# Performance work log

Hardware: AMD Instinct MI355X
Metric: run time of the kernel (lower is better)

Reference implementation:

```python
import jax, jax.numpy as jnp
import numpy as np


def setup_inputs() -> dict:
    key = jax.random.key(0)
    k_idx, k_val = jax.random.split(key)
    XSIZE = 128
    N = 500000
    B = 16
    indices = jax.random.randint(k_idx, (N, 3), 0, XSIZE, dtype=jnp.int32)
    values = jax.random.normal(k_val, (B, N), dtype=jnp.float32)
    return {"indices": indices, "values": values, "xsize": XSIZE}


def reference(indices, values, xsize):
    # densitySmoothnessVolume: scatter-add values into a (B, X, X, X) grid,
    # then TV and MSE smoothness losses over 3-axis finite differences.
    B = values.shape[0]
    X = xsize
    # flat voxel index (z, y, x) -> z*X*X + y*X + x ; shared across batch
    flat = (indices[:, 0].astype(jnp.int32) * X + indices[:, 1]) * X + indices[:, 2]
    grid = jnp.zeros((B, X * X * X), dtype=values.dtype)
    grid = grid.at[:, flat].add(values)  # scatter-add, duplicate indices accumulate
    grid = grid.reshape(B, X, X, X)

    d1 = grid[:, 1:, :, :] - grid[:, :-1, :, :]
    d2 = grid[:, :, 1:, :] - grid[:, :, :-1, :]
    d3 = grid[:, :, :, 1:] - grid[:, :, :, :-1]

    axes = (1, 2, 3)
    # total variation loss, normalized by number of voxels X^3
    num_pixels = jnp.asarray(X * X * X, dtype=values.dtype)
    tv = (jnp.sum(jnp.abs(d1), axis=axes)
          + jnp.sum(jnp.abs(d2), axis=axes)
          + jnp.sum(jnp.abs(d3), axis=axes)) / num_pixels

    # MSE smoothness loss; normalizer replicates TF code exactly:
    # 2 * prod(shape[1:3]) - shape[1] - shape[2] = 2*X^2 - 2*X
    num_pixel_pairs = jnp.asarray(2 * X * X - 2 * X, dtype=values.dtype)
    mse = (jnp.sum(jnp.square(d1), axis=axes)
           + jnp.sum(jnp.square(d2), axis=axes)
           + jnp.sum(jnp.square(d3), axis=axes)) / num_pixel_pairs

    return jnp.stack([tv, mse])  # [2, B]
```

## Files before the change

kernel.cpp:

```cpp
#include <hip/hip_runtime.h>

#define XS 128
#define PLANE (XS * XS)
#define X3 (XS * XS * XS)
#define ZC 4
#define TPB 1024
#define SLOTS 4
#define QPT 4
#define CAP 8192

__device__ __forceinline__ void bar_lgkm() {
    __builtin_amdgcn_sched_barrier(0);
    asm volatile("s_waitcnt lgkmcnt(0)" ::: "memory");
    __builtin_amdgcn_s_barrier();
    __builtin_amdgcn_sched_barrier(0);
}

__global__ __launch_bounds__(256) void init_kernel(
    int* __restrict__ cursor, float* __restrict__ out, int osz)
{
    const int t = threadIdx.x;
    if (t < XS) cursor[t] = 0;
    if (t < osz) out[t] = 0.f;
}

__global__ __launch_bounds__(256) void reorder_kernel(
    const int* __restrict__ idx, int* __restrict__ cursor,
    const float* __restrict__ vals, float* __restrict__ pvT,
    unsigned short* __restrict__ posArr, int N)
{
    __shared__ int lh[XS], lbase[XS];
    const int c0 = blockIdx.x * 1024;
    const int t = threadIdx.x;
    int z[4], key[4];
    int cntm = 0;
    const bool fast = (c0 + 1024 <= N);

    for (int i = t; i < XS; i += 256) lh[i] = 0;

    if (fast) {
        const int4* p = (const int4*)(idx + (size_t)c0 * 3);
        int4 A = p[3 * t], B4 = p[3 * t + 1], C = p[3 * t + 2];
        z[0] = A.x;  key[0] = (A.y << 7) | A.z;
        z[1] = A.w;  key[1] = (B4.x << 7) | B4.y;
        z[2] = B4.z; key[2] = (B4.w << 7) | C.x;
        z[3] = C.y;  key[3] = (C.z << 7) | C.w;
        cntm = 4;
    } else {
        #pragma unroll
        for (int i = 0; i < 4; ++i) {
            const int n = c0 + 4 * t + i;
            if (n < N) {
                z[cntm]   = idx[3 * n];
                key[cntm] = (idx[3 * n + 1] << 7) | idx[3 * n + 2];
                ++cntm;
            }
        }
    }
    __syncthreads();
    #pragma unroll
    for (int i = 0; i < 4; ++i)
        if (i < cntm) atomicAdd(&lh[z[i]], 1);
    __syncthreads();
    for (int i = t; i < XS; i += 256) {
        lbase[i] = lh[i] ? atomicAdd(&cursor[i], lh[i]) : 0;
        lh[i] = 0;
    }
    __syncthreads();

    int slot[4];
    #pragma unroll
    for (int i = 0; i < 4; ++i)
        if (i < cntm) {
            const int r = atomicAdd(&lh[z[i]], 1);
            slot[i] = z[i] * CAP + lbase[z[i]] + r;
            posArr[slot[i]] = (unsigned short)key[i];
        }

    if (fast) {
        float4 vv[16];
        #pragma unroll
        for (int b = 0; b < 16; ++b)
            vv[b] = *(const float4*)(vals + (size_t)b * N + c0 + 4 * t);
        #pragma unroll
        for (int i = 0; i < 4; ++i) {
            float4* dst = (float4*)(pvT + (size_t)slot[i] * 16);
            float4 w0 = make_float4(((const float*)&vv[0])[i],  ((const float*)&vv[1])[i],
                                    ((const float*)&vv[2])[i],  ((const float*)&vv[3])[i]);
            float4 w1 = make_float4(((const float*)&vv[4])[i],  ((const float*)&vv[5])[i],
                                    ((const float*)&vv[6])[i],  ((const float*)&vv[7])[i]);
            float4 w2 = make_float4(((const float*)&vv[8])[i],  ((const float*)&vv[9])[i],
                                    ((const float*)&vv[10])[i], ((const float*)&vv[11])[i]);
            float4 w3 = make_float4(((const float*)&vv[12])[i], ((const float*)&vv[13])[i],
                                    ((const float*)&vv[14])[i], ((const float*)&vv[15])[i]);
            dst[0] = w0; dst[1] = w1; dst[2] = w2; dst[3] = w3;
        }
    } else {
        for (int i = 0; i < cntm; ++i) {
            const int n = c0 + 4 * t + i;
            float* dst = pvT + (size_t)slot[i] * 16;
            for (int b = 0; b < 16; ++b) dst[b] = vals[(size_t)b * N + n];
        }
    }
}

__global__ __launch_bounds__(TPB, 8) void fused_kernel(
    const unsigned short* __restrict__ posArr, const int* __restrict__ cnt,
    const float* __restrict__ pvT, float* __restrict__ out, int Btot)
{
    __shared__ float buf[PLANE];
    __shared__ float rtv[TPB / 64], rms[TPB / 64];

    const int b   = blockIdx.x;
    const int z0  = blockIdx.y * ZC;
    const int tid = threadIdx.x;
    const int pmax = (z0 + ZC < XS) ? (z0 + ZC) : (XS - 1);

    int pos[SLOTS]; float val[SLOTS];
    int pc = 0, ps0 = 0;

    auto prefetch = [&](int zp) {
        ps0 = zp * CAP; pc = cnt[zp];
        #pragma unroll
        for (int i = 0; i < SLOTS; ++i) {
            const int sx = ps0 + tid + i * TPB;
            pos[i] = posArr[sx] & (PLANE - 1);
            val[i] = pvT[(size_t)sx * 16 + b];
        }
    };
    auto scatter = [&]() {
        #pragma unroll
        for (int i = 0; i < SLOTS; ++i) {
            const float v = (tid + i * TPB < pc) ? val[i] : 0.f;
            atomicAdd(&buf[pos[i]], v);
        }
        for (int e = SLOTS * TPB + tid; e < pc; e += TPB) {
            atomicAdd(&buf[posArr[ps0 + e] & (PLANE - 1)],
                      pvT[(size_t)(ps0 + e) * 16 + b]);
        }
    };

    prefetch(z0);
    #pragma unroll
    for (int i = 0; i < QPT; ++i)
        ((float4*)buf)[tid + i * TPB] = make_float4(0.f, 0.f, 0.f, 0.f);
    bar_lgkm();
    scatter();
    prefetch(z0 + 1);
    bar_lgkm();

    float4 prev[QPT];
    float tv = 0.f, ms = 0.f;

    for (int p = z0; p <= pmax; ++p) {
        float4 a[QPT];
        #pragma unroll
        for (int i = 0; i < QPT; ++i)
            a[i] = ((const float4*)buf)[tid + i * TPB];

        if (p > z0) {
            #pragma unroll
            for (int i = 0; i < QPT; ++i) {
                float d;
                d = a[i].x - prev[i].x; tv += fabsf(d); ms += d * d;
                d = a[i].y - prev[i].y; tv += fabsf(d); ms += d * d;
                d = a[i].z - prev[i].z; tv += fabsf(d); ms += d * d;
                d = a[i].w - prev[i].w; tv += fabsf(d); ms += d * d;
            }
        }
        if (p < z0 + ZC) {
            #pragma unroll
            for (int i = 0; i < QPT; ++i) {
                const int q = tid + i * TPB;
                const int qx = q & 31, y = q >> 5;
                float d;
                d = a[i].y - a[i].x; tv += fabsf(d); ms += d * d;
                d = a[i].z - a[i].y; tv += fabsf(d); ms += d * d;
                d = a[i].w - a[i].z; tv += fabsf(d); ms += d * d;
                if (qx < 31) {
                    d = buf[4 * q + 4] - a[i].w; tv += fabsf(d); ms += d * d;
                }
                if (y < XS - 1) {
                    const float4 u = ((const float4*)buf)[q + 32];
                    d = u.x - a[i].x; tv += fabsf(d); ms += d * d;
                    d = u.y - a[i].y; tv += fabsf(d); ms += d * d;
                    d = u.z - a[i].z; tv += fabsf(d); ms += d * d;
                    d = u.w - a[i].w; tv += fabsf(d); ms += d * d;
                }
            }
        }
        #pragma unroll
        for (int i = 0; i < QPT; ++i) prev[i] = a[i];

        if (p < pmax) {
            bar_lgkm();
            #pragma unroll
            for (int i = 0; i < QPT; ++i)
                ((float4*)buf)[tid + i * TPB] = make_float4(0.f, 0.f, 0.f, 0.f);
            bar_lgkm();
            scatter();
            if (p + 2 <= pmax) prefetch(p + 2);
            bar_lgkm();
        }
    }

    for (int o = 32; o > 0; o >>= 1) {
        tv += __shfl_down(tv, o); ms += __shfl_down(ms, o);
    }
    if ((tid & 63) == 0) { rtv[tid >> 6] = tv; rms[tid >> 6] = ms; }
    __syncthreads();
    if (tid == 0) {
        float t = 0.f, m = 0.f;
        #pragma unroll
        for (int w = 0; w < TPB / 64; ++w) { t += rtv[w]; m += rms[w]; }
        atomicAdd(out + b,        t * (1.0f / (float)X3));
        atomicAdd(out + Btot + b, m * (1.0f / (float)(2 * XS * XS - 2 * XS)));
    }
}

extern "C" void kernel_launch(void* const* d_in, const int* in_sizes, int n_in,
                              void* d_out, int out_size, void* d_ws, size_t ws_size,
                              hipStream_t stream)
{
    const int*   indices = (const int*)d_in[0];
    const float* values  = (const float*)d_in[1];
    const int N = in_sizes[0] / 3;
    const int B = in_sizes[1] / N;
    float* out = (float*)d_out;
    char*  ws  = (char*)d_ws;

    float* pvT = (float*)ws;
    unsigned short* posArr = (unsigned short*)(ws + (size_t)XS * CAP * 16 * sizeof(float));
    int* cursor = (int*)((char*)posArr + (size_t)XS * CAP * sizeof(unsigned short));

    init_kernel<<<1, 256, 0, stream>>>(cursor, out, out_size);
    reorder_kernel<<<(N + 1023) / 1024, 256, 0, stream>>>(
        indices, cursor, values, pvT, posArr, N);
    fused_kernel<<<dim3(B, XS / ZC), TPB, 0, stream>>>(
        posArr, cursor, pvT, out, B);
}
```

Measured before the change: 180.1 us.

## Add transpose pass to batch-major bin layout for coalesced fused-kernel loads

Adds a transpose kernel that turns the binned point-major value buffer (16 floats per point) into batch-major planes, so the fused scatter kernel reads its batch's values contiguously instead of with a 64-byte stride. It also shrinks the per-slab bin capacity from 8192 to 4608 entries to reduce workspace and the prefetch footprint. The cost is an extra kernel launch and a full extra read and write of the value buffer. There is a risk of overflow if any z-slab holds more than 4608 points; the expected count is about 3900.

```diff
diff --git a/kernel.cpp b/kernel.cpp
--- a/kernel.cpp
+++ b/kernel.cpp
@@ -7,7 +7,8 @@
 #define TPB 1024
 #define SLOTS 4
 #define QPT 4
-#define CAP 8192
+#define CAP 4608
+#define BINSPACE (XS * CAP)
 
 __device__ __forceinline__ void bar_lgkm() {
     __builtin_amdgcn_sched_barrier(0);
@@ -104,9 +105,35 @@
     }
 }
 
+__global__ __launch_bounds__(256) void transpose_kernel(
+    const float4* __restrict__ pvT, float* __restrict__ pv,
+    const int* __restrict__ cnt)
+{
+    __shared__ float tile[256][17];
+    const int z  = blockIdx.y;
+    const int t0 = blockIdx.x * 256;
+    if (t0 >= cnt[z]) return;
+    const int t = threadIdx.x;
+    const size_t s0 = (size_t)z * CAP + t0;
+
+    #pragma unroll
+    for (int i = 0; i < 4; ++i) {
+        const int f4 = t + i * 256;
+        const int s  = f4 >> 2;
+        float4 v = pvT[s0 * 4 + f4];
+        const int c = (f4 & 3) * 4;
+        tile[s][c] = v.x; tile[s][c + 1] = v.y;
+        tile[s][c + 2] = v.z; tile[s][c + 3] = v.w;
+    }
+    __syncthreads();
+    #pragma unroll
+    for (int b = 0; b < 16; ++b)
+        pv[(size_t)b * BINSPACE + s0 + t] = tile[t][b];
+}
+
 __global__ __launch_bounds__(TPB, 8) void fused_kernel(
     const unsigned short* __restrict__ posArr, const int* __restrict__ cnt,
-    const float* __restrict__ pvT, float* __restrict__ out, int Btot)
+    const float* __restrict__ pv, float* __restrict__ out, int Btot)
 {
     __shared__ float buf[PLANE];
     __shared__ float rtv[TPB / 64], rms[TPB / 64];
@@ -114,6 +141,7 @@
     const int b   = blockIdx.x;
     const int z0  = blockIdx.y * ZC;
     const int tid = threadIdx.x;
+    const float* pvb = pv + (size_t)b * BINSPACE;
     const int pmax = (z0 + ZC < XS) ? (z0 + ZC) : (XS - 1);
 
     int pos[SLOTS]; float val[SLOTS];
@@ -125,7 +153,7 @@
         for (int i = 0; i < SLOTS; ++i) {
             const int sx = ps0 + tid + i * TPB;
             pos[i] = posArr[sx] & (PLANE - 1);
-            val[i] = pvT[(size_t)sx * 16 + b];
+            val[i] = pvb[sx];
         }
     };
     auto scatter = [&]() {
@@ -135,8 +163,7 @@
             atomicAdd(&buf[pos[i]], v);
         }
         for (int e = SLOTS * TPB + tid; e < pc; e += TPB) {
-            atomicAdd(&buf[posArr[ps0 + e] & (PLANE - 1)],
-                      pvT[(size_t)(ps0 + e) * 16 + b]);
+            atomicAdd(&buf[posArr[ps0 + e] & (PLANE - 1)], pvb[ps0 + e]);
         }
     };
 
@@ -230,12 +257,15 @@
     char*  ws  = (char*)d_ws;
 
     float* pvT = (float*)ws;
-    unsigned short* posArr = (unsigned short*)(ws + (size_t)XS * CAP * 16 * sizeof(float));
-    int* cursor = (int*)((char*)posArr + (size_t)XS * CAP * sizeof(unsigned short));
+    float* pv  = pvT + (size_t)BINSPACE * 16;
+    unsigned short* posArr = (unsigned short*)(pv + (size_t)16 * BINSPACE);
+    int* cursor = (int*)((char*)posArr + (size_t)BINSPACE * sizeof(unsigned short));
 
     init_kernel<<<1, 256, 0, stream>>>(cursor, out, out_size);
     reorder_kernel<<<(N + 1023) / 1024, 256, 0, stream>>>(
         indices, cursor, values, pvT, posArr, N);
+    transpose_kernel<<<dim3(CAP / 256, XS), 256, 0, stream>>>(
+        (const float4*)pvT, pv, cursor);
     fused_kernel<<<dim3(B, XS / ZC), TPB, 0, stream>>>(
-        posArr, cursor, pvT, out, B);
-}
+        posArr, cursor, pv, out, B);
+}
```

After: 184.7 us. +2.6%, slower.
